# Kernel tuning notes

Hardware: AMD Instinct MI355X
Metric: run time of the kernel (lower is better)

## Reference

```python
import jax, jax.numpy as jnp
import numpy as np

NUM_HEADS = 8
DIM = 256
MLP_RATIO = 1.2


def conv1x1(x, w, b=None):
    # x: [B,C,H,W], w: [O,C]
    y = jnp.einsum('bchw,oc->bohw', x, w)
    if b is not None:
        y = y + b[None, :, None, None]
    return y


def dwconv3x3(x, w):
    # depthwise 3x3, stride 1, padding 1. w: [C,1,3,3]
    C = x.shape[1]
    return jax.lax.conv_general_dilated(
        x, w, window_strides=(1, 1), padding=((1, 1), (1, 1)),
        dimension_numbers=('NCHW', 'OIHW', 'NCHW'), feature_group_count=C)


def l2norm(x, axis):
    # matches torch.nn.functional.normalize (eps=1e-12 clamp on the norm)
    n = jnp.sqrt(jnp.sum(x * x, axis=axis, keepdims=True))
    return x / jnp.maximum(n, 1e-12)


def setup_inputs() -> dict:
    key = jax.random.key(0)
    ks = jax.random.split(key, 7)
    dim = DIM
    hidden = int(dim * MLP_RATIO)  # 307
    B, H, W = 8, 64, 64
    return {
        'x': jax.random.normal(ks[0], (B, dim, H, W), jnp.float32),
        'w_qkv': jax.random.normal(ks[1], (3 * dim, dim), jnp.float32) * 0.02,
        'w_dw': jax.random.normal(ks[2], (3 * dim, 1, 3, 3), jnp.float32) * 0.1,
        'temperature': jnp.ones((NUM_HEADS, 1, 1), jnp.float32),
        'w_proj': jax.random.normal(ks[3], (dim, dim), jnp.float32) * 0.02,
        'w_mlp1': jax.random.normal(ks[4], (hidden, dim), jnp.float32) * 0.02,
        'b_mlp1': jnp.zeros((hidden,), jnp.float32),
        'w_mlp2': jax.random.normal(ks[5], (dim, hidden), jnp.float32) * 0.02,
        'b_mlp2': jnp.zeros((dim,), jnp.float32),
    }


def reference(x, w_qkv, w_dw, temperature, w_proj, w_mlp1, b_mlp1, w_mlp2, b_mlp2):
    b, c, h, w = x.shape
    head = NUM_HEADS
    # MDTA attention: qkv 1x1 conv -> depthwise 3x3 conv
    qkv = dwconv3x3(conv1x1(x, w_qkv), w_dw)          # [B,3C,H,W]
    q, k, v = jnp.split(qkv, 3, axis=1)
    to_heads = lambda t: t.reshape(b, head, c // head, h * w)  # b head c (h w)
    q, k, v = to_heads(q), to_heads(k), to_heads(v)
    q = l2norm(q, -1)
    k = l2norm(k, -1)
    # channel-wise (transposed) attention: [B,head,c_h,c_h]
    attn = jnp.einsum('bhcn,bhdn->bhcd', q, k) * temperature[None]
    attn = jax.nn.softmax(attn, axis=-1)
    out = jnp.einsum('bhcd,bhdn->bhcn', attn, v).reshape(b, c, h, w)
    x = x + conv1x1(out, w_proj)                       # residual 1
    # conv-FFN (1x1 -> GELU -> 1x1) with residual
    y = jax.nn.gelu(conv1x1(x, w_mlp1, b_mlp1))
    x = x + conv1x1(y, w_mlp2, b_mlp2)                 # residual 2
    return x
```

## Files before the change

### kernel.cpp

```cpp
#include <hip/hip_runtime.h>
#include <hip/hip_bf16.h>
#include <math.h>

typedef __hip_bfloat16 bf16;
using s16x8 = __attribute__((ext_vector_type(8))) short;
using f32x4 = __attribute__((ext_vector_type(4))) float;

#define B_ 8
#define C_ 256
#define HW_ 4096
#define TC_ 768
#define NH_ 8
#define CH_ 32
#define HID_ 307
#define HIDP_ 320
#define HIDM_ 384

__device__ __forceinline__ float ldf(const float* p) { return *p; }
__device__ __forceinline__ float ldf(const bf16* p)  { return __bfloat162float(*p); }
__device__ __forceinline__ void  stf(float* p, float v) { *p = v; }
__device__ __forceinline__ void  stf(bf16* p, float v)  { *p = __float2bfloat16(v); }

__device__ __forceinline__ float bfu2f(unsigned short u) {
    union { unsigned int i; float f; } c; c.i = ((unsigned int)u) << 16; return c.f;
}

__device__ __forceinline__ float gelu_tanh(float u) {
    float c = 0.7978845608028654f * (u + 0.044715f * u * u * u);
    return 0.5f * u * (1.f + tanhf(c));
}

__device__ __forceinline__ void stage16(const void* g, uint32_t* lbase, int lane) {
#if __has_builtin(__builtin_amdgcn_global_load_lds)
    __builtin_amdgcn_global_load_lds(
        (const __attribute__((address_space(1))) uint32_t*)g,
        (__attribute__((address_space(3))) uint32_t*)lbase, 16, 0, 0);
#else
    ((uint4*)lbase)[lane] = *(const uint4*)g;
#endif
}

template <typename TOut>
__global__ __launch_bounds__(256) void mfma_gemm(
    const bf16* __restrict__ A, const bf16* __restrict__ Xt,
    const float* __restrict__ bias, const float* __restrict__ res,
    TOut* __restrict__ out, int M, int Nld, int Nw, int Kp, int act,
    int bias_on_n, int bias_len,
    size_t astride, size_t xstride, size_t ostride)
{
    int bt = blockIdx.z;
    A  += (size_t)bt * astride;
    Xt += (size_t)bt * xstride;
    out += (size_t)bt * ostride;
    if (res) res += (size_t)bt * ostride;
    int m0 = blockIdx.y * 128, n0 = blockIdx.x * 128;

    __shared__ uint32_t lds[8192];

    int tid = threadIdx.x;
    int w = tid >> 6, lane = tid & 63;
    int wr = w >> 1, wc = w & 1;
    int r15 = lane & 15, g = lane >> 4;

    f32x4 zero4 = {0.f, 0.f, 0.f, 0.f};
    f32x4 acc[4][4];
    #pragma unroll
    for (int i = 0; i < 4; i++)
        #pragma unroll
        for (int j = 0; j < 4; j++) acc[i][j] = zero4;

    int nkt = Kp >> 6;
    for (int kt = 0; kt < nkt; kt++) {
        #pragma unroll
        for (int i = 0; i < 4; i++) {
            int row = (w * 4 + i) * 8 + (lane >> 3);
            int us  = (lane & 7) ^ (row & 7);
            const bf16* sa = A  + (size_t)(m0 + row) * Kp + kt * 64 + us * 8;
            const bf16* sb = Xt + (size_t)(n0 + row) * Kp + kt * 64 + us * 8;
            stage16(sa, &lds[(w * 4 + i) * 256], lane);
            stage16(sb, &lds[4096 + (w * 4 + i) * 256], lane);
        }
        __syncthreads();

        s16x8 af[4][2], bfr[4][2];
        #pragma unroll
        for (int mm = 0; mm < 4; mm++) {
            int r = wr * 64 + mm * 16 + r15;
            #pragma unroll
            for (int ks = 0; ks < 2; ks++) {
                int u = (ks * 4 + g) ^ (r & 7);
                af[mm][ks] = *(const s16x8*)&lds[(unsigned)(r * 8 + u) * 4];
            }
        }
        #pragma unroll
        for (int nn = 0; nn < 4; nn++) {
            int r = wc * 64 + nn * 16 + r15;
            #pragma unroll
            for (int ks = 0; ks < 2; ks++) {
                int u = (ks * 4 + g) ^ (r & 7);
                bfr[nn][ks] = *(const s16x8*)&lds[4096 + (unsigned)(r * 8 + u) * 4];
            }
        }

        #pragma unroll
        for (int ks = 0; ks < 2; ks++)
            #pragma unroll
            for (int mm = 0; mm < 4; mm++)
                #pragma unroll
                for (int nn = 0; nn < 4; nn++)
                    acc[mm][nn] = __builtin_amdgcn_mfma_f32_16x16x32_bf16(
                        af[mm][ks], bfr[nn][ks], acc[mm][nn], 0, 0, 0);
        __syncthreads();
    }

    #pragma unroll
    for (int mm = 0; mm < 4; mm++) {
        int mbase = m0 + wr * 64 + mm * 16 + g * 4;
        #pragma unroll
        for (int rr = 0; rr < 4; rr++) {
            int m = mbase + rr;
            if (m >= M) continue;
            float bvm = (bias && !bias_on_n) ? bias[m] : 0.f;
            #pragma unroll
            for (int nn = 0; nn < 4; nn++) {
                int n = n0 + wc * 64 + nn * 16 + r15;
                if (n >= Nw) continue;
                float bv = bias_on_n ? ((bias && n < bias_len) ? bias[n] : 0.f) : bvm;
                float v = acc[mm][nn][rr] + bv;
                if (act == 1) v = gelu_tanh(v);
                if (res) v += res[(size_t)m * Nld + n];
                stf(&out[(size_t)m * Nld + n], v);
            }
        }
    }
}

template <typename TIn>
__global__ __launch_bounds__(256) void transpose_kernel(
    const TIn* __restrict__ in, bf16* __restrict__ out,
    int R, int Ncols, int Rpad, size_t in_z, size_t out_z)
{
    in  += (size_t)blockIdx.z * in_z;
    out += (size_t)blockIdx.z * out_z;
    __shared__ float t[32][33];
    int r0 = blockIdx.y * 32, n0 = blockIdx.x * 32;
    int tx = threadIdx.x & 31, ty = threadIdx.x >> 5;
    #pragma unroll
    for (int s = 0; s < 4; s++) {
        int r = r0 + ty + 8 * s;
        t[ty + 8 * s][tx] = (r < R) ? ldf(&in[(size_t)r * Ncols + n0 + tx]) : 0.f;
    }
    __syncthreads();
    #pragma unroll
    for (int s = 0; s < 4; s++) {
        int n = n0 + ty + 8 * s;
        out[(size_t)n * Rpad + r0 + tx] = __float2bfloat16(t[tx][ty + 8 * s]);
    }
}

__global__ __launch_bounds__(256) void convert_pad_kernel(
    const float* __restrict__ in, bf16* __restrict__ out,
    int R, int Cin, int Cout)
{
    int c = blockIdx.x * 256 + threadIdx.x;
    int r = blockIdx.y;
    if (c >= Cout) return;
    float v = (r < R && c < Cin) ? in[(size_t)r * Cin + c] : 0.f;
    out[(size_t)r * Cout + c] = __float2bfloat16(v);
}

__global__ __launch_bounds__(256) void dwconv_kernel(
    const bf16* __restrict__ in, const float* __restrict__ wdw,
    bf16* __restrict__ out)
{
    int plane = blockIdx.x;
    int c = plane % TC_;
    const bf16* ip = in + ((size_t)plane << 12);
    bf16*       op = out + ((size_t)plane << 12);

    __shared__ bf16 sp[64][72];

    int t = threadIdx.x;
    #pragma unroll
    for (int i = 0; i < 2; i++) {
        int px = (t + 256 * i) * 8;
        int r = px >> 6, col = px & 63;
        *(uint4*)&sp[r][col] = *(const uint4*)&ip[px];
    }
    float w[9];
    #pragma unroll
    for (int k = 0; k < 9; k++) w[k] = wdw[c * 9 + k];
    __syncthreads();

    int row = t >> 2, c0 = (t & 3) * 16;
    float acc[16];
    #pragma unroll
    for (int j = 0; j < 16; j++) acc[j] = 0.f;

    #pragma unroll
    for (int dy = -1; dy <= 1; dy++) {
        int yy = row + dy;
        if (yy < 0 || yy > 63) continue;
        float vals[18];
        vals[0]  = (c0 > 0)       ? __bfloat162float(sp[yy][c0 - 1])  : 0.f;
        s16x8 v0 = *(const s16x8*)&sp[yy][c0];
        s16x8 v1 = *(const s16x8*)&sp[yy][c0 + 8];
        #pragma unroll
        for (int j = 0; j < 8; j++) {
            vals[j + 1] = bfu2f((unsigned short)v0[j]);
            vals[j + 9] = bfu2f((unsigned short)v1[j]);
        }
        vals[17] = (c0 + 16 < 64) ? __bfloat162float(sp[yy][c0 + 16]) : 0.f;
        float w0 = w[(dy + 1) * 3], w1 = w[(dy + 1) * 3 + 1], w2 = w[(dy + 1) * 3 + 2];
        #pragma unroll
        for (int j = 0; j < 16; j++)
            acc[j] += w0 * vals[j] + w1 * vals[j + 1] + w2 * vals[j + 2];
    }

    bf16 ob[16];
    #pragma unroll
    for (int j = 0; j < 16; j++) ob[j] = __float2bfloat16(acc[j]);
    #pragma unroll
    for (int i = 0; i < 2; i++)
        *(uint4*)&op[row * 64 + c0 + i * 8] = *(uint4*)&ob[i * 8];
}

__global__ void zero_kernel(float* __restrict__ p, int n)
{
    int i = blockIdx.x * 256 + threadIdx.x;
    if (i < n) p[i] = 0.f;
}

__global__ __launch_bounds__(256) void qk_partial_kernel(
    const bf16* __restrict__ qkv, float* __restrict__ S,
    float* __restrict__ n2q, float* __restrict__ n2k)
{
    int bh = blockIdx.y;
    int b = bh >> 3, h = bh & 7;
    int base = blockIdx.x * 512;
    const bf16* qp = qkv + ((size_t)b * TC_ + h * CH_) * HW_;
    const bf16* kp = qp + (size_t)C_ * HW_;

    __shared__ float qs[32][65], ks[32][65];

    int tid = threadIdx.x;
    int nr = tid >> 3, seg = (tid & 7) * 8;
    float accA[4] = {0.f, 0.f, 0.f, 0.f};
    float sq = 0.f, sk = 0.f;

    for (int t0 = 0; t0 < 512; t0 += 64) {
        #pragma unroll
        for (int i = 0; i < 8; i++) {
            int l = tid + 256 * i;
            int r = l >> 6, cc = l & 63;
            qs[r][cc] = __bfloat162float(qp[(size_t)r * HW_ + base + t0 + cc]);
            ks[r][cc] = __bfloat162float(kp[(size_t)r * HW_ + base + t0 + cc]);
        }
        __syncthreads();
        #pragma unroll
        for (int p = 0; p < 4; p++) {
            int e = tid + 256 * p;
            int i = e >> 5, j = e & 31;
            float s = 0.f;
            #pragma unroll
            for (int kk = 0; kk < 64; kk++) s += qs[i][kk] * ks[j][kk];
            accA[p] += s;
        }
        #pragma unroll
        for (int s = 0; s < 8; s++) {
            float vq = qs[nr][seg + s]; sq += vq * vq;
            float vk = ks[nr][seg + s]; sk += vk * vk;
        }
        __syncthreads();
    }

    #pragma unroll
    for (int off = 1; off < 8; off <<= 1) {
        sq += __shfl_xor(sq, off);
        sk += __shfl_xor(sk, off);
    }
    if ((tid & 7) == 0) {
        atomicAdd(&n2q[bh * 32 + nr], sq);
        atomicAdd(&n2k[bh * 32 + nr], sk);
    }
    #pragma unroll
    for (int p = 0; p < 4; p++) {
        int e = tid + 256 * p;
        atomicAdd(&S[(size_t)bh * 1024 + e], accA[p]);
    }
}

__global__ __launch_bounds__(64) void softmax_kernel(
    const float* __restrict__ S, const float* __restrict__ n2q,
    const float* __restrict__ n2k, const float* __restrict__ temp,
    float* __restrict__ attnb)
{
    int bh = blockIdx.x, h = bh & 7;
    __shared__ float nkl[32];
    int tid = threadIdx.x;
    if (tid < 32) nkl[tid] = fmaxf(sqrtf(n2k[bh * 32 + tid]), 1e-12f);
    __syncthreads();
    if (tid < 32) {
        float nq = fmaxf(sqrtf(n2q[bh * 32 + tid]), 1e-12f);
        float tp = temp[h];
        float row[32];
        float m = -1e30f;
        #pragma unroll
        for (int j = 0; j < 32; j++) {
            row[j] = S[(size_t)bh * 1024 + tid * 32 + j] * tp / (nq * nkl[j]);
            m = fmaxf(m, row[j]);
        }
        float s = 0.f;
        #pragma unroll
        for (int j = 0; j < 32; j++) { row[j] = expf(row[j] - m); s += row[j]; }
        float inv = 1.f / s;
        #pragma unroll
        for (int j = 0; j < 32; j++)
            attnb[(size_t)bh * 1024 + tid * 32 + j] = row[j] * inv;
    }
}

__global__ __launch_bounds__(256) void wcomb_kernel(
    const float* __restrict__ w_proj, const float* __restrict__ attnb,
    bf16* __restrict__ wcomb)
{
    int bh = blockIdx.x;
    int b = bh >> 3, h = bh & 7;
    __shared__ float at[32][33];
    int tid = threadIdx.x;
    #pragma unroll
    for (int p = 0; p < 4; p++) {
        int e = tid + 256 * p;
        at[e >> 5][e & 31] = attnb[(size_t)bh * 1024 + e];
    }
    __syncthreads();
    int m = tid;
    float wrow[32];
    #pragma unroll
    for (int i = 0; i < 32; i++) wrow[i] = w_proj[(size_t)m * C_ + h * 32 + i];
    #pragma unroll
    for (int j = 0; j < 32; j++) {
        float s = 0.f;
        #pragma unroll
        for (int i = 0; i < 32; i++) s += wrow[i] * at[i][j];
        wcomb[((size_t)b * C_ + m) * C_ + h * 32 + j] = __float2bfloat16(s);
    }
}

extern "C" void kernel_launch(void* const* d_in, const int* in_sizes, int n_in,
                              void* d_out, int out_size, void* d_ws, size_t ws_size,
                              hipStream_t stream)
{
    const float* x      = (const float*)d_in[0];
    const float* w_qkv  = (const float*)d_in[1];
    const float* w_dw   = (const float*)d_in[2];
    const float* temp   = (const float*)d_in[3];
    const float* w_proj = (const float*)d_in[4];
    const float* w_mlp1 = (const float*)d_in[5];
    const float* b_mlp1 = (const float*)d_in[6];
    const float* w_mlp2 = (const float*)d_in[7];
    const float* b_mlp2 = (const float*)d_in[8];

    char* ws = (char*)d_ws;
    bf16*  qkv_pre = (bf16*)ws;
    bf16*  xt      = (bf16*)(ws + (size_t)50331648);
    bf16*  wqkv_bf = (bf16*)(ws + (size_t)67108864);
    bf16*  qkv     = (bf16*)(ws + (size_t)50331648);
    float* x2      = (float*)ws;
    float* S_f     = (float*)(ws + (size_t)33554432);
    float* n2q     = S_f + 65536;
    float* n2k     = n2q + 2048;
    float* attnb   = n2k + 2048;
    bf16*  wcomb   = (bf16*)(ws + (size_t)34095104);
    bf16*  wm1_bf  = (bf16*)(ws + (size_t)35143680);
    bf16*  wm2_bf  = (bf16*)(ws + (size_t)35438592);
    bf16*  vt      = (bf16*)(ws + (size_t)35602432);
    bf16*  x2t     = (bf16*)(ws + (size_t)52379648);
    bf16*  yt      = (bf16*)(ws + (size_t)72400896);

    convert_pad_kernel<<<dim3(1, TC_), 256, 0, stream>>>(w_qkv, wqkv_bf, TC_, C_, C_);
    transpose_kernel<float><<<dim3(128, 8, B_), 256, 0, stream>>>(
        x, xt, C_, HW_, C_, (size_t)C_ * HW_, (size_t)HW_ * C_);

    mfma_gemm<bf16><<<dim3(32, 6, B_), 256, 0, stream>>>(
        wqkv_bf, xt, nullptr, nullptr, qkv_pre, TC_, HW_, HW_, C_, 0, 0, 0,
        0, (size_t)HW_ * C_, (size_t)TC_ * HW_);

    dwconv_kernel<<<B_ * TC_, 256, 0, stream>>>(qkv_pre, w_dw, qkv);

    zero_kernel<<<(69632 + 255) / 256, 256, 0, stream>>>(S_f, 69632);
    qk_partial_kernel<<<dim3(8, 64), 256, 0, stream>>>(qkv, S_f, n2q, n2k);
    softmax_kernel<<<64, 64, 0, stream>>>(S_f, n2q, n2k, temp, attnb);
    wcomb_kernel<<<64, 256, 0, stream>>>(w_proj, attnb, wcomb);

    convert_pad_kernel<<<dim3(1, HIDM_), 256, 0, stream>>>(w_mlp1, wm1_bf, HID_, C_, C_);
    convert_pad_kernel<<<dim3(2, C_), 256, 0, stream>>>(w_mlp2, wm2_bf, C_, HID_, HIDP_);
    transpose_kernel<bf16><<<dim3(128, 8, B_), 256, 0, stream>>>(
        qkv + (size_t)2 * C_ * HW_, vt, C_, HW_, C_,
        (size_t)TC_ * HW_, (size_t)HW_ * C_);

    mfma_gemm<float><<<dim3(32, 2, B_), 256, 0, stream>>>(
        wcomb, vt, nullptr, x, x2, C_, HW_, HW_, C_, 0, 0, 0,
        (size_t)C_ * C_, (size_t)HW_ * C_, (size_t)C_ * HW_);

    transpose_kernel<float><<<dim3(128, 8, B_), 256, 0, stream>>>(
        x2, x2t, C_, HW_, C_, (size_t)C_ * HW_, (size_t)HW_ * C_);

    mfma_gemm<bf16><<<dim3(3, 32, B_), 256, 0, stream>>>(
        x2t, wm1_bf, b_mlp1, nullptr, yt, HW_, HIDP_, HIDP_, C_, 1, 1, HID_,
        (size_t)HW_ * C_, 0, (size_t)HW_ * HIDP_);

    mfma_gemm<float><<<dim3(32, 2, B_), 256, 0, stream>>>(
        wm2_bf, yt, b_mlp2, x2, (float*)d_out, C_, HW_, HW_, HIDP_, 0, 0, 0,
        0, (size_t)HW_ * HIDP_, (size_t)C_ * HW_);
}
```

Measured before the change: 377.7 us.

## Fuse both MLP GEMMs into one kernel keeping GELU hidden activations in LDS

Replaces the two separate MLP GEMM launches with a single kernel. For each 64-pixel tile it computes the first projection, applies bias and tanh-GELU, and stores the hidden tile in shared memory, then runs the second projection with bias and residual straight from that buffer. This removes the global write and re-read of the bf16 hidden tensor and one kernel launch. In exchange, weight fragments are loaded directly from global memory (relying on L2) with no LDS staging, and the 42KB of LDS per block may limit occupancy. The unused bias-on-N path is also stripped from the generic GEMM.

Result: slower. 507.4 us (+34.3%).

```diff
diff --git a/kernel.cpp b/kernel.cpp
--- a/kernel.cpp
+++ b/kernel.cpp
@@ -45,7 +45,6 @@
     const bf16* __restrict__ A, const bf16* __restrict__ Xt,
     const float* __restrict__ bias, const float* __restrict__ res,
     TOut* __restrict__ out, int M, int Nld, int Nw, int Kp, int act,
-    int bias_on_n, int bias_len,
     size_t astride, size_t xstride, size_t ostride)
 {
     int bt = blockIdx.z;
@@ -120,18 +119,129 @@
         for (int rr = 0; rr < 4; rr++) {
             int m = mbase + rr;
             if (m >= M) continue;
-            float bvm = (bias && !bias_on_n) ? bias[m] : 0.f;
+            float bvm = bias ? bias[m] : 0.f;
             #pragma unroll
             for (int nn = 0; nn < 4; nn++) {
                 int n = n0 + wc * 64 + nn * 16 + r15;
                 if (n >= Nw) continue;
-                float bv = bias_on_n ? ((bias && n < bias_len) ? bias[n] : 0.f) : bvm;
-                float v = acc[mm][nn][rr] + bv;
+                float v = acc[mm][nn][rr] + bvm;
                 if (act == 1) v = gelu_tanh(v);
                 if (res) v += res[(size_t)m * Nld + n];
                 stf(&out[(size_t)m * Nld + n], v);
             }
         }
+    }
+}
+
+__global__ __launch_bounds__(256) void mlp_fused(
+    const bf16* __restrict__ x2t, const bf16* __restrict__ wm1,
+    const float* __restrict__ b1, const bf16* __restrict__ wm2,
+    const float* __restrict__ b2, const float* __restrict__ res,
+    float* __restrict__ out)
+{
+    int b = blockIdx.y;
+    int p0 = blockIdx.x * 64;
+    x2t += (size_t)b * HW_ * C_;
+    res += (size_t)b * C_ * HW_;
+    out += (size_t)b * C_ * HW_;
+
+    __shared__ bf16 h[64][328];
+
+    int tid = threadIdx.x;
+    int w = tid >> 6, lane = tid & 63;
+    int wr = w >> 1, wc = w & 1;
+    int r15 = lane & 15, g = lane >> 4;
+
+    f32x4 zero4 = {0.f, 0.f, 0.f, 0.f};
+
+    s16x8 bx[8][2];
+    #pragma unroll
+    for (int kt = 0; kt < 8; kt++)
+        #pragma unroll
+        for (int nn = 0; nn < 2; nn++) {
+            int px = p0 + wc * 32 + nn * 16 + r15;
+            bx[kt][nn] = *(const s16x8*)&x2t[(size_t)px * C_ + kt * 32 + g * 8];
+        }
+
+    #pragma unroll
+    for (int mt = 0; mt < 3; mt++) {
+        f32x4 acc[4][2];
+        #pragma unroll
+        for (int mm = 0; mm < 4; mm++)
+            #pragma unroll
+            for (int nn = 0; nn < 2; nn++) acc[mm][nn] = zero4;
+
+        #pragma unroll
+        for (int kt = 0; kt < 8; kt++) {
+            s16x8 a[4];
+            #pragma unroll
+            for (int mm = 0; mm < 4; mm++) {
+                int hid = mt * 128 + wr * 64 + mm * 16 + r15;
+                a[mm] = *(const s16x8*)&wm1[(size_t)hid * C_ + kt * 32 + g * 8];
+            }
+            #pragma unroll
+            for (int mm = 0; mm < 4; mm++)
+                #pragma unroll
+                for (int nn = 0; nn < 2; nn++)
+                    acc[mm][nn] = __builtin_amdgcn_mfma_f32_16x16x32_bf16(
+                        a[mm], bx[kt][nn], acc[mm][nn], 0, 0, 0);
+        }
+        #pragma unroll
+        for (int mm = 0; mm < 4; mm++)
+            #pragma unroll
+            for (int nn = 0; nn < 2; nn++)
+                #pragma unroll
+                for (int rr = 0; rr < 4; rr++) {
+                    int hid = mt * 128 + wr * 64 + mm * 16 + g * 4 + rr;
+                    int px = wc * 32 + nn * 16 + r15;
+                    if (hid < HIDP_) {
+                        float v = 0.f;
+                        if (hid < HID_) v = gelu_tanh(acc[mm][nn][rr] + b1[hid]);
+                        h[px][hid] = __float2bfloat16(v);
+                    }
+                }
+    }
+    __syncthreads();
+
+    #pragma unroll
+    for (int mt = 0; mt < 2; mt++) {
+        f32x4 acc[4][2];
+        #pragma unroll
+        for (int mm = 0; mm < 4; mm++)
+            #pragma unroll
+            for (int nn = 0; nn < 2; nn++) acc[mm][nn] = zero4;
+
+        #pragma unroll
+        for (int kt = 0; kt < 10; kt++) {
+            s16x8 a[4], bh[2];
+            #pragma unroll
+            for (int mm = 0; mm < 4; mm++) {
+                int c = mt * 128 + wr * 64 + mm * 16 + r15;
+                a[mm] = *(const s16x8*)&wm2[(size_t)c * HIDP_ + kt * 32 + g * 8];
+            }
+            #pragma unroll
+            for (int nn = 0; nn < 2; nn++)
+                bh[nn] = *(const s16x8*)&h[wc * 32 + nn * 16 + r15][kt * 32 + g * 8];
+            #pragma unroll
+            for (int mm = 0; mm < 4; mm++)
+                #pragma unroll
+                for (int nn = 0; nn < 2; nn++)
+                    acc[mm][nn] = __builtin_amdgcn_mfma_f32_16x16x32_bf16(
+                        a[mm], bh[nn], acc[mm][nn], 0, 0, 0);
+        }
+        #pragma unroll
+        for (int mm = 0; mm < 4; mm++)
+            #pragma unroll
+            for (int rr = 0; rr < 4; rr++) {
+                int c = mt * 128 + wr * 64 + mm * 16 + g * 4 + rr;
+                float bv = b2[c];
+                #pragma unroll
+                for (int nn = 0; nn < 2; nn++) {
+                    int px = p0 + wc * 32 + nn * 16 + r15;
+                    out[(size_t)c * HW_ + px] =
+                        acc[mm][nn][rr] + bv + res[(size_t)c * HW_ + px];
+                }
+            }
     }
 }
 
@@ -376,14 +486,13 @@
     bf16*  wm2_bf  = (bf16*)(ws + (size_t)35438592);
     bf16*  vt      = (bf16*)(ws + (size_t)35602432);
     bf16*  x2t     = (bf16*)(ws + (size_t)52379648);
-    bf16*  yt      = (bf16*)(ws + (size_t)72400896);
 
     convert_pad_kernel<<<dim3(1, TC_), 256, 0, stream>>>(w_qkv, wqkv_bf, TC_, C_, C_);
     transpose_kernel<float><<<dim3(128, 8, B_), 256, 0, stream>>>(
         x, xt, C_, HW_, C_, (size_t)C_ * HW_, (size_t)HW_ * C_);
 
     mfma_gemm<bf16><<<dim3(32, 6, B_), 256, 0, stream>>>(
-        wqkv_bf, xt, nullptr, nullptr, qkv_pre, TC_, HW_, HW_, C_, 0, 0, 0,
+        wqkv_bf, xt, nullptr, nullptr, qkv_pre, TC_, HW_, HW_, C_, 0,
         0, (size_t)HW_ * C_, (size_t)TC_ * HW_);
 
     dwconv_kernel<<<B_ * TC_, 256, 0, stream>>>(qkv_pre, w_dw, qkv);
@@ -400,17 +509,12 @@
         (size_t)TC_ * HW_, (size_t)HW_ * C_);
 
     mfma_gemm<float><<<dim3(32, 2, B_), 256, 0, stream>>>(
-        wcomb, vt, nullptr, x, x2, C_, HW_, HW_, C_, 0, 0, 0,
+        wcomb, vt, nullptr, x, x2, C_, HW_, HW_, C_, 0,
         (size_t)C_ * C_, (size_t)HW_ * C_, (size_t)C_ * HW_);
 
     transpose_kernel<float><<<dim3(128, 8, B_), 256, 0, stream>>>(
         x2, x2t, C_, HW_, C_, (size_t)C_ * HW_, (size_t)HW_ * C_);
 
-    mfma_gemm<bf16><<<dim3(3, 32, B_), 256, 0, stream>>>(
-        x2t, wm1_bf, b_mlp1, nullptr, yt, HW_, HIDP_, HIDP_, C_, 1, 1, HID_,
-        (size_t)HW_ * C_, 0, (size_t)HW_ * HIDP_);
-
-    mfma_gemm<float><<<dim3(32, 2, B_), 256, 0, stream>>>(
-        wm2_bf, yt, b_mlp2, x2, (float*)d_out, C_, HW_, HW_, HIDP_, 0, 0, 0,
-        0, (size_t)HW_ * HIDP_, (size_t)C_ * HW_);
-}
+    mlp_fused<<<dim3(HW_ / 64, B_), 256, 0, stream>>>(
+        x2t, wm1_bf, b_mlp1, wm2_bf, b_mlp2, x2, (float*)d_out);
+}
```

## Double-buffer GEMM LDS staging and fuse x2 transpose into projection epilogue

Applied to the files above, without the earlier changes.

The MFMA GEMM now uses two LDS buffers and prefetches the next K tile while computing the current one, leaving one barrier per iteration. The projection GEMM also writes a transposed bf16 copy of its output, which removes the separate x2 transpose kernel. The MLP1 GEMM is then launched as a single batch over all 32768 rows. The costs are doubled LDS per block, which may lower occupancy, and scattered 2-byte transposed stores in the epilogue.

New measurement: 480.1 us. +27.1%, slower.

```diff
diff --git a/kernel.cpp b/kernel.cpp
--- a/kernel.cpp
+++ b/kernel.cpp
@@ -45,17 +45,18 @@
     const bf16* __restrict__ A, const bf16* __restrict__ Xt,
     const float* __restrict__ bias, const float* __restrict__ res,
     TOut* __restrict__ out, int M, int Nld, int Nw, int Kp, int act,
-    int bias_on_n, int bias_len,
-    size_t astride, size_t xstride, size_t ostride)
+    int bias_on_n, int bias_len, bf16* __restrict__ outT,
+    size_t astride, size_t xstride, size_t ostride, size_t otstride)
 {
     int bt = blockIdx.z;
     A  += (size_t)bt * astride;
     Xt += (size_t)bt * xstride;
     out += (size_t)bt * ostride;
-    if (res) res += (size_t)bt * ostride;
+    if (res)  res  += (size_t)bt * ostride;
+    if (outT) outT += (size_t)bt * otstride;
     int m0 = blockIdx.y * 128, n0 = blockIdx.x * 128;
 
-    __shared__ uint32_t lds[8192];
+    __shared__ uint32_t lds[16384];
 
     int tid = threadIdx.x;
     int w = tid >> 6, lane = tid & 63;
@@ -70,18 +71,35 @@
         for (int j = 0; j < 4; j++) acc[i][j] = zero4;
 
     int nkt = Kp >> 6;
+    int srow = (w * 4) * 8 + (lane >> 3);
+
+    #pragma unroll
+    for (int i = 0; i < 4; i++) {
+        int row = srow + i * 8;
+        int us  = (lane & 7) ^ (row & 7);
+        stage16(A  + (size_t)(m0 + row) * Kp + us * 8, &lds[(w * 4 + i) * 256], lane);
+        stage16(Xt + (size_t)(n0 + row) * Kp + us * 8, &lds[4096 + (w * 4 + i) * 256], lane);
+    }
+    asm volatile("s_waitcnt vmcnt(0)" ::: "memory");
+    __syncthreads();
+
+    int cur = 0;
     for (int kt = 0; kt < nkt; kt++) {
-        #pragma unroll
-        for (int i = 0; i < 4; i++) {
-            int row = (w * 4 + i) * 8 + (lane >> 3);
-            int us  = (lane & 7) ^ (row & 7);
-            const bf16* sa = A  + (size_t)(m0 + row) * Kp + kt * 64 + us * 8;
-            const bf16* sb = Xt + (size_t)(n0 + row) * Kp + kt * 64 + us * 8;
-            stage16(sa, &lds[(w * 4 + i) * 256], lane);
-            stage16(sb, &lds[4096 + (w * 4 + i) * 256], lane);
-        }
-        __syncthreads();
-
+        int nb = cur ^ 1;
+        if (kt + 1 < nkt) {
+            #pragma unroll
+            for (int i = 0; i < 4; i++) {
+                int row = srow + i * 8;
+                int us  = (lane & 7) ^ (row & 7);
+                stage16(A  + (size_t)(m0 + row) * Kp + (kt + 1) * 64 + us * 8,
+                        &lds[nb * 8192 + (w * 4 + i) * 256], lane);
+                stage16(Xt + (size_t)(n0 + row) * Kp + (kt + 1) * 64 + us * 8,
+                        &lds[nb * 8192 + 4096 + (w * 4 + i) * 256], lane);
+            }
+        }
+
+        const uint32_t* la = &lds[cur * 8192];
+        const uint32_t* lb = &lds[cur * 8192 + 4096];
         s16x8 af[4][2], bfr[4][2];
         #pragma unroll
         for (int mm = 0; mm < 4; mm++) {
@@ -89,7 +107,7 @@
             #pragma unroll
             for (int ks = 0; ks < 2; ks++) {
                 int u = (ks * 4 + g) ^ (r & 7);
-                af[mm][ks] = *(const s16x8*)&lds[(unsigned)(r * 8 + u) * 4];
+                af[mm][ks] = *(const s16x8*)&la[(unsigned)(r * 8 + u) * 4];
             }
         }
         #pragma unroll
@@ -98,7 +116,7 @@
             #pragma unroll
             for (int ks = 0; ks < 2; ks++) {
                 int u = (ks * 4 + g) ^ (r & 7);
-                bfr[nn][ks] = *(const s16x8*)&lds[4096 + (unsigned)(r * 8 + u) * 4];
+                bfr[nn][ks] = *(const s16x8*)&lb[(unsigned)(r * 8 + u) * 4];
             }
         }
 
@@ -110,7 +128,12 @@
                 for (int nn = 0; nn < 4; nn++)
                     acc[mm][nn] = __builtin_amdgcn_mfma_f32_16x16x32_bf16(
                         af[mm][ks], bfr[nn][ks], acc[mm][nn], 0, 0, 0);
-        __syncthreads();
+
+        if (kt + 1 < nkt) {
+            asm volatile("s_waitcnt vmcnt(0)" ::: "memory");
+            __syncthreads();
+        }
+        cur = nb;
     }
 
     #pragma unroll
@@ -130,6 +153,7 @@
                 if (act == 1) v = gelu_tanh(v);
                 if (res) v += res[(size_t)m * Nld + n];
                 stf(&out[(size_t)m * Nld + n], v);
+                if (outT) outT[(size_t)n * M + m] = __float2bfloat16(v);
             }
         }
     }
@@ -383,8 +407,8 @@
         x, xt, C_, HW_, C_, (size_t)C_ * HW_, (size_t)HW_ * C_);
 
     mfma_gemm<bf16><<<dim3(32, 6, B_), 256, 0, stream>>>(
-        wqkv_bf, xt, nullptr, nullptr, qkv_pre, TC_, HW_, HW_, C_, 0, 0, 0,
-        0, (size_t)HW_ * C_, (size_t)TC_ * HW_);
+        wqkv_bf, xt, nullptr, nullptr, qkv_pre, TC_, HW_, HW_, C_, 0, 0, 0, nullptr,
+        0, (size_t)HW_ * C_, (size_t)TC_ * HW_, 0);
 
     dwconv_kernel<<<B_ * TC_, 256, 0, stream>>>(qkv_pre, w_dw, qkv);
 
@@ -400,17 +424,14 @@
         (size_t)TC_ * HW_, (size_t)HW_ * C_);
 
     mfma_gemm<float><<<dim3(32, 2, B_), 256, 0, stream>>>(
-        wcomb, vt, nullptr, x, x2, C_, HW_, HW_, C_, 0, 0, 0,
-        (size_t)C_ * C_, (size_t)HW_ * C_, (size_t)C_ * HW_);
-
-    transpose_kernel<float><<<dim3(128, 8, B_), 256, 0, stream>>>(
-        x2, x2t, C_, HW_, C_, (size_t)C_ * HW_, (size_t)HW_ * C_);
-
-    mfma_gemm<bf16><<<dim3(3, 32, B_), 256, 0, stream>>>(
-        x2t, wm1_bf, b_mlp1, nullptr, yt, HW_, HIDP_, HIDP_, C_, 1, 1, HID_,
-        (size_t)HW_ * C_, 0, (size_t)HW_ * HIDP_);
+        wcomb, vt, nullptr, x, x2, C_, HW_, HW_, C_, 0, 0, 0, x2t,
+        (size_t)C_ * C_, (size_t)HW_ * C_, (size_t)C_ * HW_, (size_t)HW_ * C_);
+
+    mfma_gemm<bf16><<<dim3(3, 256, 1), 256, 0, stream>>>(
+        x2t, wm1_bf, b_mlp1, nullptr, yt, 32768, HIDP_, HIDP_, C_, 1, 1, HID_, nullptr,
+        0, 0, 0, 0);
 
     mfma_gemm<float><<<dim3(32, 2, B_), 256, 0, stream>>>(
-        wm2_bf, yt, b_mlp2, x2, (float*)d_out, C_, HW_, HW_, HIDP_, 0, 0, 0,
-        0, (size_t)HW_ * HIDP_, (size_t)C_ * HW_);
-}
+        wm2_bf, yt, b_mlp2, x2, (float*)d_out, C_, HW_, HW_, HIDP_, 0, 0, 0, nullptr,
+        0, (size_t)HW_ * HIDP_, (size_t)C_ * HW_, 0);
+}
```
